# Kernel tuning notes

Hardware: AMD Instinct MI355X
Metric: run time of the kernel (lower is better)

The kernel has to match this reference:

```python
import jax, jax.numpy as jnp
import numpy as np

B, T, F_DIM, HID, CH = 16, 4096, 47, 64, 256  # batch, frames, feature_dim, hidden_feature_dim, num_channels


def setup_inputs() -> dict:
    key = jax.random.key(0)
    ks = jax.random.split(key, 8)
    s = 0.08  # weight scale
    return {
        "features": jax.random.normal(ks[0], (B, T, F_DIM), jnp.float32),
        # conv1: Conv1d(47, 64, k=1) -> pointwise linear, torch weight (out,in,1) squeezed
        "W1": jax.random.normal(ks[1], (HID, F_DIM), jnp.float32) * s,
        "b1": jnp.zeros((HID,), jnp.float32),
        # conv2: Conv1d(256, 256, k=2), torch weight (out, in, k)
        "W2": jax.random.normal(ks[2], (CH, 4 * HID, 2), jnp.float32) * s,
        "b2": jnp.zeros((CH,), jnp.float32),
        # tconv: ConvTranspose1d(256, 256, k=4, stride=4), torch weight (in, out, k)
        "Wt": jax.random.normal(ks[3], (CH, CH, 4), jnp.float32) * s,
        "bt": jnp.zeros((CH,), jnp.float32),
        # GRU(256, 256), torch layout: (3*H, in) with gate order [r, z, n]
        "W_ih": jax.random.normal(ks[4], (3 * CH, CH), jnp.float32) * s,
        "W_hh": jax.random.normal(ks[5], (3 * CH, CH), jnp.float32) * s,
        "b_ih": jnp.zeros((3 * CH,), jnp.float32),
        "b_hh": jnp.zeros((3 * CH,), jnp.float32),
    }


def reference(features, W1, b1, W2, b2, Wt, bt, W_ih, W_hh, b_ih, b_hh):
    b, t = features.shape[0], features.shape[1]
    ch = Wt.shape[1]
    # conv1 (k=1) == pointwise linear + tanh: (B,T,47) -> (B,T,64)
    c = jnp.tanh(jnp.einsum('btf,hf->bth', features, W1) + b1)
    # group 4 frames: (B, T/4, 256)
    c = c.reshape(b, t // 4, -1)
    # conv2 k=2 with left pad 1 (causal): y[t] = W2[..0] x[t-1] + W2[..1] x[t]
    cp = jnp.pad(c, ((0, 0), (1, 0), (0, 0)))
    c = jnp.tanh(jnp.einsum('bti,oi->bto', cp[:, :-1], W2[:, :, 0])
                 + jnp.einsum('bti,oi->bto', cp[:, 1:], W2[:, :, 1]) + b2)
    # tconv: stride-4 transpose conv, k=4 -> each frame emits 4 steps
    c = jnp.tanh(jnp.einsum('bti,iok->btko', c, Wt) + bt)  # (B, T/4, 4, CH)
    c = c.reshape(b, t, ch)
    # GRU (torch semantics, gate order r,z,n); precompute input projections
    gates_x = jnp.einsum('btc,gc->btg', c, W_ih) + b_ih  # (B,T,3CH)

    def step(h, gx):
        gh = h @ W_hh.T + b_hh
        xr, xz, xn = jnp.split(gx, 3, axis=-1)
        hr, hz, hn = jnp.split(gh, 3, axis=-1)
        r = jax.nn.sigmoid(xr + hr)
        z = jax.nn.sigmoid(xz + hz)
        n = jnp.tanh(xn + r * hn)
        h = (1 - z) * n + z * h
        return h, h

    h0 = jnp.zeros((b, ch), features.dtype)
    _, hs = jax.lax.scan(step, h0, jnp.swapaxes(gates_x, 0, 1))  # (T,B,CH)
    return jnp.swapaxes(hs, 0, 1)  # (B,T,CH)
```

## Files before the change

kernel.cpp:

```cpp
#include <hip/hip_runtime.h>
#include <hip/hip_bf16.h>
#include <stdint.h>

#define B_   16
#define T_   4096
#define F_   47
#define HID_ 64
#define CH_  256
#define TG_  1024
#define G3_  768

using bf16x8 = __attribute__((ext_vector_type(8))) short;
using f32x4  = __attribute__((ext_vector_type(4))) float;
using f16x8  = __attribute__((ext_vector_type(8))) _Float16;
using h2     = __attribute__((ext_vector_type(2))) _Float16;

__device__ __forceinline__ short f2bf(float f) {
    union { float f; uint32_t u; } v; v.f = f;
    uint32_t u = v.u;
    uint32_t r = (u + 0x7fffu + ((u >> 16) & 1u)) >> 16;
    return (short)r;
}
__device__ __forceinline__ float bf2f(short s) {
    union { uint32_t u; float f; } v; v.u = ((uint32_t)(uint16_t)s) << 16;
    return v.f;
}
__device__ __forceinline__ float fast_tanh(float x) {
    float e = __expf(2.f * x);
    return 1.f - 2.f / (e + 1.f);
}
__device__ __forceinline__ float fast_sigmoid(float x) {
    return 1.f / (1.f + __expf(-x));
}

#if __has_builtin(__builtin_amdgcn_fdot2)
#define FDOT2(a, b, c) __builtin_amdgcn_fdot2((a), (b), (c), false)
#else
__device__ __forceinline__ float fdot2_emul(h2 a, h2 b, float c) {
    return c + (float)a[0] * (float)b[0] + (float)a[1] * (float)b[1];
}
#define FDOT2(a, b, c) fdot2_emul((a), (b), (c))
#endif

#if __has_builtin(__builtin_amdgcn_global_load_lds)
#define HAS_GLL 1
__device__ __forceinline__ void gl_lds16(const void* g, void* l) {
    __builtin_amdgcn_global_load_lds(
        (const __attribute__((address_space(1))) uint32_t*)g,
        (__attribute__((address_space(3))) uint32_t*)l, 16, 0, 0);
}
#else
#define HAS_GLL 0
#endif

__global__ __launch_bounds__(256) void k1_conv1(const float* __restrict__ feat,
        const float* __restrict__ W1, const float* __restrict__ b1,
        short* __restrict__ c1) {
    __shared__ float sW[47 * 64];
    __shared__ float sF[4 * 47];
    int tid = threadIdx.x;
    int b = blockIdx.x >> 10, t0 = (blockIdx.x & 1023) * 4;
    if (tid < 188) sF[tid] = feat[((size_t)b * T_ + t0) * 47 + tid];
    for (int i = tid; i < 47 * 64; i += 256) {
        int f = i >> 6, h = i & 63;
        sW[i] = W1[h * 47 + f];
    }
    __syncthreads();
    int fr = tid >> 6, h = tid & 63;
    float acc = b1[h];
    #pragma unroll
    for (int f = 0; f < 47; ++f)
        acc += sF[fr * 47 + f] * sW[f * 64 + h];
    c1[((size_t)b * T_ + t0 + fr) * 64 + h] = f2bf(fast_tanh(acc));
}

__global__ __launch_bounds__(256) void k_prep(const float* __restrict__ W2,
        const float* __restrict__ Wt, const float* __restrict__ Wih_f,
        short* __restrict__ W2t, short* __restrict__ Wtt, short* __restrict__ Wih) {
    int idx = blockIdx.x * 256 + threadIdx.x;
    if (idx < 256 * 512) {
        int o = idx >> 9, i = idx & 511, d = i >> 8, jj = i & 255;
        W2t[idx] = f2bf(W2[(size_t)o * 512 + jj * 2 + d]);
    }
    {
        int n = idx >> 8, ic = idx & 255, o = n & 255, kp = n >> 8;
        Wtt[idx] = f2bf(Wt[(size_t)ic * 1024 + o * 4 + kp]);
    }
    if (idx < G3_ * CH_)
        Wih[idx] = f2bf(Wih_f[idx]);
}

__global__ __launch_bounds__(256) void k2_conv2(const short* __restrict__ c1,
        const short* __restrict__ W2t, const float* __restrict__ b2,
        short* __restrict__ y2) {
    int tid = threadIdx.x, w = tid >> 6, l = tid & 63;
    int lane16 = l & 15, quad = l >> 4;
    int mt = blockIdx.x * 4 + w;
    int row = mt * 16 + lane16;
    int tg = row & 1023;
    const short* Arow = c1 + (size_t)row * 256 - 256;
    bf16x8 zero8 = {0,0,0,0,0,0,0,0};
    bf16x8 af[16];
    #pragma unroll
    for (int kt = 0; kt < 16; ++kt) {
        int i0 = kt * 32 + quad * 8;
        bool masked = (tg == 0) && (kt < 8);
        const short* p = masked ? c1 : (Arow + i0);
        bf16x8 v = *(const bf16x8*)p;
        af[kt] = masked ? zero8 : v;
    }
    #pragma unroll
    for (int nt = 0; nt < 16; ++nt) {
        int n = nt * 16 + lane16;
        f32x4 acc = {0.f, 0.f, 0.f, 0.f};
        const short* Brow = W2t + (size_t)n * 512 + quad * 8;
        #pragma unroll
        for (int kt = 0; kt < 16; ++kt) {
            bf16x8 bf = *(const bf16x8*)(Brow + kt * 32);
            acc = __builtin_amdgcn_mfma_f32_16x16x32_bf16(af[kt], bf, acc, 0, 0, 0);
        }
        float bias = b2[n];
        #pragma unroll
        for (int r = 0; r < 4; ++r) {
            int mrow = mt * 16 + quad * 4 + r;
            y2[(size_t)mrow * 256 + n] = f2bf(fast_tanh(acc[r] + bias));
        }
    }
}

__global__ __launch_bounds__(256) void k3a_tconv(const short* __restrict__ y2,
        const short* __restrict__ Wtt, const float* __restrict__ bt,
        short* __restrict__ c3) {
    int tid = threadIdx.x, w = tid >> 6, l = tid & 63;
    int lane16 = l & 15, quad = l >> 4;
    int mt = blockIdx.x;
    int row = mt * 16 + lane16;
    const short* Arow = y2 + (size_t)row * 256 + quad * 8;
    bf16x8 af[8];
    #pragma unroll
    for (int kt = 0; kt < 8; ++kt) af[kt] = *(const bf16x8*)(Arow + kt * 32);
    #pragma unroll
    for (int nt2 = 0; nt2 < 16; ++nt2) {
        int n = (w * 16 + nt2) * 16 + lane16;
        f32x4 acc = {0.f, 0.f, 0.f, 0.f};
        const short* Brow = Wtt + (size_t)n * 256 + quad * 8;
        #pragma unroll
        for (int kt = 0; kt < 8; ++kt) {
            bf16x8 bf = *(const bf16x8*)(Brow + kt * 32);
            acc = __builtin_amdgcn_mfma_f32_16x16x32_bf16(af[kt], bf, acc, 0, 0, 0);
        }
        int kp = n >> 8, o = n & 255;
        float bias = bt[o];
        #pragma unroll
        for (int r = 0; r < 4; ++r) {
            int mrow = mt * 16 + quad * 4 + r;
            int bb = mrow >> 10, tgg = mrow & 1023;
            c3[(((size_t)bb * TG_ + tgg) * 4 + kp) * 256 + o] =
                f2bf(fast_tanh(acc[r] + bias));
        }
    }
}

__global__ __launch_bounds__(256) void k3b_xproj(const short* __restrict__ c3,
        const short* __restrict__ Wih, const float* __restrict__ b_ih,
        short* __restrict__ gates) {
    int tid = threadIdx.x, w = tid >> 6, l = tid & 63;
    int lane16 = l & 15, quad = l >> 4;
    int mt = blockIdx.x;
    int row = mt * 16 + lane16;
    const short* Arow = c3 + (size_t)row * 256 + quad * 8;
    bf16x8 af[8];
    #pragma unroll
    for (int kt = 0; kt < 8; ++kt) af[kt] = *(const bf16x8*)(Arow + kt * 32);
    #pragma unroll
    for (int nt2 = 0; nt2 < 12; ++nt2) {
        int n = (w * 12 + nt2) * 16 + lane16;
        f32x4 acc = {0.f, 0.f, 0.f, 0.f};
        const short* Brow = Wih + (size_t)n * 256 + quad * 8;
        #pragma unroll
        for (int kt = 0; kt < 8; ++kt) {
            bf16x8 bf = *(const bf16x8*)(Brow + kt * 32);
            acc = __builtin_amdgcn_mfma_f32_16x16x32_bf16(af[kt], bf, acc, 0, 0, 0);
        }
        float bias = b_ih[n];
        #pragma unroll
        for (int r = 0; r < 4; ++r) {
            int mrow = mt * 16 + quad * 4 + r;
            gates[(size_t)mrow * G3_ + n] = f2bf(acc[r] + bias);
        }
    }
}

__global__ __launch_bounds__(512) void k4_gru_dot2(const float* __restrict__ W_hh,
        const float* __restrict__ b_hh, const short* __restrict__ gates,
        float* __restrict__ out) {
    __shared__ __align__(16) short gxb[2][8][G3_];
    __shared__ __align__(16) float part[G3_ * 4];
    __shared__ __align__(16) float ob[8 * 256];
    __shared__ __align__(16) short hq_s[4 * 72];

    int tid = threadIdx.x, l = tid & 63, w = tid >> 6;
    int q = tid & 3, n0 = tid >> 2;
    int b = blockIdx.x;

    h2 wreg[6][32];
    #pragma unroll
    for (int k = 0; k < 6; ++k) {
        const float2* row = (const float2*)(W_hh + ((size_t)(n0 + k * 128)) * 256 + q * 64);
        #pragma unroll
        for (int j = 0; j < 32; ++j) {
            float2 v = row[j];
            h2 p; p[0] = (_Float16)v.x; p[1] = (_Float16)v.y;
            wreg[k][j] = p;
        }
    }

    float h_reg = 0.f, bhr = 0.f, bhz = 0.f, bhn = 0.f;
    if (tid < 256) {
        bhr = b_hh[tid]; bhz = b_hh[256 + tid]; bhn = b_hh[512 + tid];
    }
    if (tid < 288) hq_s[tid] = 0;

    const short* gbase = gates + (size_t)b * T_ * G3_;
    const char* gbytes = (const char*)gbase;

#if HAS_GLL
    {
        char* dst = (char*)&gxb[0][0][0];
        gl_lds16(gbytes + w * 1024 + l * 16, dst + w * 1024);
        if (w < 4) gl_lds16(gbytes + (8 + w) * 1024 + l * 16, dst + (8 + w) * 1024);
    }
#else
    {
        const uint32_t* g32 = (const uint32_t*)gbytes;
        uint32_t* d = (uint32_t*)&gxb[0][0][0];
        #pragma unroll
        for (int i = 0; i < 6; ++i) d[tid + i * 512] = g32[tid + i * 512];
    }
#endif
    __syncthreads();

    float* outb = out + (size_t)b * T_ * CH_;
    for (int s = 0; s < T_; ++s) {
        bool grp0 = ((s & 7) == 0) && (s + 8 < T_);
#if HAS_GLL
        if (grp0) {
            const char* src = gbytes + (size_t)(s + 8) * 1536;
            char* dst = (char*)&gxb[((s >> 3) + 1) & 1][0][0];
            gl_lds16(src + w * 1024 + l * 16, dst + w * 1024);
            if (w < 4) gl_lds16(src + (8 + w) * 1024 + l * 16, dst + (8 + w) * 1024);
        }
#else
        uint32_t pf[6];
        if (grp0) {
            const uint32_t* src = (const uint32_t*)(gbytes + (size_t)(s + 8) * 1536);
            #pragma unroll
            for (int i = 0; i < 6; ++i) pf[i] = src[tid + i * 512];
        }
#endif

        h2 hq[32];
        #pragma unroll
        for (int g2 = 0; g2 < 8; ++g2) {
            f16x8 v = *(const f16x8*)&hq_s[q * 72 + g2 * 8];
            #pragma unroll
            for (int p2 = 0; p2 < 4; ++p2) {
                h2 p; p[0] = v[p2 * 2]; p[1] = v[p2 * 2 + 1];
                hq[g2 * 4 + p2] = p;
            }
        }
        float acc[6] = {0.f, 0.f, 0.f, 0.f, 0.f, 0.f};
        #pragma unroll
        for (int j = 0; j < 32; ++j) {
            #pragma unroll
            for (int k = 0; k < 6; ++k)
                acc[k] = FDOT2(wreg[k][j], hq[j], acc[k]);
        }
        #pragma unroll
        for (int k = 0; k < 6; ++k)
            part[(n0 + k * 128) * 4 + q] = acc[k];
        __syncthreads();

#if !HAS_GLL
        if (grp0) {
            uint32_t* d = (uint32_t*)&gxb[((s >> 3) + 1) & 1][0][0];
            #pragma unroll
            for (int i = 0; i < 6; ++i) d[tid + i * 512] = pf[i];
        }
#endif
        if (tid < 256) {
            const short* gx = &gxb[(s >> 3) & 1][s & 7][0];
            f32x4 pr = *(const f32x4*)&part[tid * 4];
            f32x4 pz = *(const f32x4*)&part[(256 + tid) * 4];
            f32x4 pn = *(const f32x4*)&part[(512 + tid) * 4];
            float gr = (pr[0] + pr[1]) + (pr[2] + pr[3]);
            float gz = (pz[0] + pz[1]) + (pz[2] + pz[3]);
            float gn = (pn[0] + pn[1]) + (pn[2] + pn[3]);
            float xr = bf2f(gx[tid]), xz = bf2f(gx[256 + tid]), xn = bf2f(gx[512 + tid]);
            float r = fast_sigmoid(xr + gr + bhr);
            float z = fast_sigmoid(xz + gz + bhz);
            float nn = fast_tanh(xn + r * (gn + bhn));
            h_reg = (1.f - z) * nn + z * h_reg;
            union { _Float16 f; short u; } cv; cv.f = (_Float16)h_reg;
            hq_s[(tid >> 6) * 72 + (tid & 63)] = cv.u;
            ob[(s & 7) * 256 + tid] = h_reg;
        }
        __syncthreads();

        if ((s & 7) == 7) {
            f32x4 v = *(const f32x4*)&ob[tid * 4];
            *(f32x4*)&outb[(size_t)(s - 7 + (tid >> 6)) * 256 + (tid & 63) * 4] = v;
        }
    }
}

extern "C" void kernel_launch(void* const* d_in, const int* in_sizes, int n_in,
                              void* d_out, int out_size, void* d_ws, size_t ws_size,
                              hipStream_t stream) {
    const float* feat  = (const float*)d_in[0];
    const float* W1    = (const float*)d_in[1];
    const float* b1    = (const float*)d_in[2];
    const float* W2    = (const float*)d_in[3];
    const float* b2    = (const float*)d_in[4];
    const float* Wt    = (const float*)d_in[5];
    const float* bt    = (const float*)d_in[6];
    const float* Wih_f = (const float*)d_in[7];
    const float* Whh   = (const float*)d_in[8];
    const float* bih   = (const float*)d_in[9];
    const float* bhh   = (const float*)d_in[10];
    float* out = (float*)d_out;

    char* ws = (char*)d_ws;
    short* c3    = (short*)(ws);
    short* c1    = (short*)(ws);
    short* gates = (short*)(ws + 33554432);
    short* y2    = (short*)(ws + 33554432);
    short* W2t   = (short*)(ws + 134217728);
    short* Wtt   = (short*)(ws + 134217728 + 262144);
    short* Wih   = (short*)(ws + 134217728 + 262144 + 524288);

    k1_conv1   <<<16384, 256, 0, stream>>>(feat, W1, b1, c1);
    k_prep     <<<1024, 256, 0, stream>>>(W2, Wt, Wih_f, W2t, Wtt, Wih);
    k2_conv2   <<<256,  256, 0, stream>>>(c1, W2t, b2, y2);
    k3a_tconv  <<<1024, 256, 0, stream>>>(y2, Wtt, bt, c3);
    k3b_xproj  <<<4096, 256, 0, stream>>>(c3, Wih, bih, gates);
    k4_gru_dot2<<<16,   512, 0, stream>>>(Whh, bhh, gates, out);
}
```

Measured before the change: 5.223 ms.

## Split GRU recurrence K-dimension across 1024 threads with 8-way partial sums

```diff
diff --git a/kernel.cpp b/kernel.cpp
--- a/kernel.cpp
+++ b/kernel.cpp
@@ -12,6 +12,7 @@
 
 using bf16x8 = __attribute__((ext_vector_type(8))) short;
 using f32x4  = __attribute__((ext_vector_type(4))) float;
+using f32x2  = __attribute__((ext_vector_type(2))) float;
 using f16x8  = __attribute__((ext_vector_type(8))) _Float16;
 using h2     = __attribute__((ext_vector_type(2))) _Float16;
 
@@ -191,24 +192,24 @@
     }
 }
 
-__global__ __launch_bounds__(512) void k4_gru_dot2(const float* __restrict__ W_hh,
+__global__ __launch_bounds__(1024, 4) void k4_gru_dot2(const float* __restrict__ W_hh,
         const float* __restrict__ b_hh, const short* __restrict__ gates,
         float* __restrict__ out) {
-    __shared__ __align__(16) short gxb[2][8][G3_];
-    __shared__ __align__(16) float part[G3_ * 4];
+    __shared__ __align__(16) short gxb[2][16][G3_];
+    __shared__ __align__(16) float part[8 * 776];
     __shared__ __align__(16) float ob[8 * 256];
-    __shared__ __align__(16) short hq_s[4 * 72];
-
-    int tid = threadIdx.x, l = tid & 63, w = tid >> 6;
-    int q = tid & 3, n0 = tid >> 2;
+    __shared__ __align__(16) short hq_s[8 * 40];
+
+    int tid = threadIdx.x;
+    int q = tid & 7, n0 = tid >> 3;
     int b = blockIdx.x;
 
-    h2 wreg[6][32];
+    h2 wreg[6][16];
     #pragma unroll
     for (int k = 0; k < 6; ++k) {
-        const float2* row = (const float2*)(W_hh + ((size_t)(n0 + k * 128)) * 256 + q * 64);
-        #pragma unroll
-        for (int j = 0; j < 32; ++j) {
+        const float2* row = (const float2*)(W_hh + ((size_t)(n0 + k * 128)) * 256 + q * 32);
+        #pragma unroll
+        for (int j = 0; j < 16; ++j) {
             float2 v = row[j];
             h2 p; p[0] = (_Float16)v.x; p[1] = (_Float16)v.y;
             wreg[k][j] = p;
@@ -219,97 +220,94 @@
     if (tid < 256) {
         bhr = b_hh[tid]; bhz = b_hh[256 + tid]; bhn = b_hh[512 + tid];
     }
-    if (tid < 288) hq_s[tid] = 0;
-
-    const short* gbase = gates + (size_t)b * T_ * G3_;
-    const char* gbytes = (const char*)gbase;
+    if (tid < 320) hq_s[tid] = 0;
+
+    const char* gbytes = (const char*)(gates + (size_t)b * T_ * G3_);
 
 #if HAS_GLL
     {
         char* dst = (char*)&gxb[0][0][0];
-        gl_lds16(gbytes + w * 1024 + l * 16, dst + w * 1024);
-        if (w < 4) gl_lds16(gbytes + (8 + w) * 1024 + l * 16, dst + (8 + w) * 1024);
+        gl_lds16(gbytes + tid * 16, dst + (tid >> 6) * 1024);
+        if (tid < 512)
+            gl_lds16(gbytes + 16384 + tid * 16, dst + 16384 + (tid >> 6) * 1024);
     }
 #else
     {
         const uint32_t* g32 = (const uint32_t*)gbytes;
         uint32_t* d = (uint32_t*)&gxb[0][0][0];
         #pragma unroll
-        for (int i = 0; i < 6; ++i) d[tid + i * 512] = g32[tid + i * 512];
+        for (int i = 0; i < 6; ++i) d[tid + i * 1024] = g32[tid + i * 1024];
     }
 #endif
     __syncthreads();
 
     float* outb = out + (size_t)b * T_ * CH_;
     for (int s = 0; s < T_; ++s) {
-        bool grp0 = ((s & 7) == 0) && (s + 8 < T_);
+        bool grp0 = ((s & 15) == 0) && (s + 16 < T_);
 #if HAS_GLL
         if (grp0) {
-            const char* src = gbytes + (size_t)(s + 8) * 1536;
-            char* dst = (char*)&gxb[((s >> 3) + 1) & 1][0][0];
-            gl_lds16(src + w * 1024 + l * 16, dst + w * 1024);
-            if (w < 4) gl_lds16(src + (8 + w) * 1024 + l * 16, dst + (8 + w) * 1024);
+            const char* src = gbytes + (size_t)(s + 16) * 1536;
+            char* dst = (char*)&gxb[((s >> 4) + 1) & 1][0][0];
+            gl_lds16(src + tid * 16, dst + (tid >> 6) * 1024);
+            if (tid < 512)
+                gl_lds16(src + 16384 + tid * 16, dst + 16384 + (tid >> 6) * 1024);
         }
 #else
         uint32_t pf[6];
         if (grp0) {
-            const uint32_t* src = (const uint32_t*)(gbytes + (size_t)(s + 8) * 1536);
+            const uint32_t* src = (const uint32_t*)(gbytes + (size_t)(s + 16) * 1536);
             #pragma unroll
-            for (int i = 0; i < 6; ++i) pf[i] = src[tid + i * 512];
-        }
-#endif
-
-        h2 hq[32];
-        #pragma unroll
-        for (int g2 = 0; g2 < 8; ++g2) {
-            f16x8 v = *(const f16x8*)&hq_s[q * 72 + g2 * 8];
+            for (int i = 0; i < 6; ++i) pf[i] = src[tid + i * 1024];
+        }
+#endif
+
+        float acc[6] = {0.f, 0.f, 0.f, 0.f, 0.f, 0.f};
+        #pragma unroll
+        for (int c = 0; c < 4; ++c) {
+            f16x8 v = *(const f16x8*)&hq_s[q * 40 + c * 8];
             #pragma unroll
             for (int p2 = 0; p2 < 4; ++p2) {
-                h2 p; p[0] = v[p2 * 2]; p[1] = v[p2 * 2 + 1];
-                hq[g2 * 4 + p2] = p;
+                h2 hp; hp[0] = v[p2 * 2]; hp[1] = v[p2 * 2 + 1];
+                #pragma unroll
+                for (int k = 0; k < 6; ++k)
+                    acc[k] = FDOT2(wreg[k][c * 4 + p2], hp, acc[k]);
             }
         }
-        float acc[6] = {0.f, 0.f, 0.f, 0.f, 0.f, 0.f};
-        #pragma unroll
-        for (int j = 0; j < 32; ++j) {
-            #pragma unroll
-            for (int k = 0; k < 6; ++k)
-                acc[k] = FDOT2(wreg[k][j], hq[j], acc[k]);
-        }
         #pragma unroll
         for (int k = 0; k < 6; ++k)
-            part[(n0 + k * 128) * 4 + q] = acc[k];
+            part[q * 776 + n0 + k * 128] = acc[k];
         __syncthreads();
 
 #if !HAS_GLL
         if (grp0) {
-            uint32_t* d = (uint32_t*)&gxb[((s >> 3) + 1) & 1][0][0];
+            uint32_t* d = (uint32_t*)&gxb[((s >> 4) + 1) & 1][0][0];
             #pragma unroll
-            for (int i = 0; i < 6; ++i) d[tid + i * 512] = pf[i];
+            for (int i = 0; i < 6; ++i) d[tid + i * 1024] = pf[i];
         }
 #endif
         if (tid < 256) {
-            const short* gx = &gxb[(s >> 3) & 1][s & 7][0];
-            f32x4 pr = *(const f32x4*)&part[tid * 4];
-            f32x4 pz = *(const f32x4*)&part[(256 + tid) * 4];
-            f32x4 pn = *(const f32x4*)&part[(512 + tid) * 4];
-            float gr = (pr[0] + pr[1]) + (pr[2] + pr[3]);
-            float gz = (pz[0] + pz[1]) + (pz[2] + pz[3]);
-            float gn = (pn[0] + pn[1]) + (pn[2] + pn[3]);
+            const short* gx = &gxb[(s >> 4) & 1][s & 15][0];
+            float gr = 0.f, gz = 0.f, gn = 0.f;
+            #pragma unroll
+            for (int qq = 0; qq < 8; ++qq) {
+                gr += part[qq * 776 + tid];
+                gz += part[qq * 776 + 256 + tid];
+                gn += part[qq * 776 + 512 + tid];
+            }
             float xr = bf2f(gx[tid]), xz = bf2f(gx[256 + tid]), xn = bf2f(gx[512 + tid]);
             float r = fast_sigmoid(xr + gr + bhr);
             float z = fast_sigmoid(xz + gz + bhz);
             float nn = fast_tanh(xn + r * (gn + bhn));
             h_reg = (1.f - z) * nn + z * h_reg;
             union { _Float16 f; short u; } cv; cv.f = (_Float16)h_reg;
-            hq_s[(tid >> 6) * 72 + (tid & 63)] = cv.u;
+            hq_s[(tid >> 5) * 40 + (tid & 31)] = cv.u;
             ob[(s & 7) * 256 + tid] = h_reg;
         }
         __syncthreads();
 
         if ((s & 7) == 7) {
-            f32x4 v = *(const f32x4*)&ob[tid * 4];
-            *(f32x4*)&outb[(size_t)(s - 7 + (tid >> 6)) * 256 + (tid & 63) * 4] = v;
+            f32x2 v = *(const f32x2*)&ob[tid * 2];
+            *(f32x2*)&outb[(size_t)(s - 7 + (tid >> 7)) * 256 + (tid & 127) * 2] = v;
         }
     }
 }
@@ -344,5 +342,5 @@
     k2_conv2   <<<256,  256, 0, stream>>>(c1, W2t, b2, y2);
     k3a_tconv  <<<1024, 256, 0, stream>>>(y2, Wtt, bt, c3);
     k3b_xproj  <<<4096, 256, 0, stream>>>(c3, Wih, bih, gates);
-    k4_gru_dot2<<<16,   512, 0, stream>>>(Whh, bhh, gates, out);
-}
+    k4_gru_dot2<<<16,  1024, 0, stream>>>(Whh, bhh, gates, out);
+}
```

Measured after the change: 5.943 ms. 13.8% more time.
